# Kernel optimization log

Measured on AMD Instinct MI355X. Metric: run time of the kernel, lower is better.

Reference implementation:

```python
import jax, jax.numpy as jnp
import numpy as np


def setup_inputs() -> dict:
    key = jax.random.key(0)
    kq, kk, kv = jax.random.split(key, 3)
    B, S, D = 8, 2048, 128
    Q = jax.random.normal(kq, (B, S, D), dtype=jnp.float32)
    K = jax.random.normal(kk, (B, S, D), dtype=jnp.float32)
    V = jax.random.normal(kv, (B, S, D), dtype=jnp.float32)
    return {"Q": Q, "K": K, "V": V}


def reference(Q, K, V):
    # scores: [B, S, S]
    d = Q.shape[-1]
    scores = jnp.einsum('bqd,bkd->bqk', Q, K) / jnp.sqrt(jnp.float32(d))
    # causal mask: position i attends to keys <= i (original sets upper triangle to -inf)
    S = scores.shape[-1]
    causal = jnp.tril(jnp.ones((S, S), dtype=bool))  # [S, S]
    scores = jnp.where(causal[None, :, :], scores, -jnp.inf)
    probs = jax.nn.softmax(scores, axis=-1)
    return jnp.einsum('bqk,bkd->bqd', probs, V)
```

## Files before the change

### kernel.cpp

```cpp
#include <hip/hip_runtime.h>

#define BB 8
#define SS 2048
#define DD 128

typedef _Float16 f16;
typedef _Float16 f16x8 __attribute__((ext_vector_type(8)));
typedef float f32x4 __attribute__((ext_vector_type(4)));

#define SWV(d) ((((d) & 7) ^ (((d) >> 3) & 7)) << 3)

static __device__ __forceinline__ unsigned short f2h(float x) {
    f16 h = (f16)x;
    return __builtin_bit_cast(unsigned short, h);
}

static __device__ __forceinline__ float fast_exp2(float x) {
#if __has_builtin(__builtin_amdgcn_exp2f)
    return __builtin_amdgcn_exp2f(x);
#else
    return exp2f(x);
#endif
}

template <int NS>
__global__ __launch_bounds__(256, 2)
void attn_fwd(const float* __restrict__ Qg, const float* __restrict__ Kg,
              const float* __restrict__ Vg, float* __restrict__ Og,
              float* __restrict__ Opart, float2* __restrict__ mlb)
{
    __shared__ __align__(16) f16 Kl[64 * 128];
    __shared__ __align__(16) f16 Vt[128 * 64];
    __shared__ __align__(16) f16 Pl[4][16 * 64];

    const int tid  = threadIdx.x;
    const int lane = tid & 63;
    const int w    = tid >> 6;
    const int c_   = lane & 15;
    const int g    = lane >> 4;

    const int L   = blockIdx.x;
    const int bb  = L & 7;
    const int rem = L >> 3;
    const int qb  = 31 - (rem / NS);
    const int s   = rem % NS;
    const int T   = qb + 1;
    const int t0  = (T * s) / NS;
    const int t1  = (T * (s + 1)) / NS;

    const int qrow0 = qb * 64 + w * 16;

    const float qs = 0.08838834764831845f * 1.4426950408889634f;
    f16x8 qf[4];
    {
        const float* qp = Qg + (size_t)(bb * SS + qrow0 + c_) * DD;
#pragma unroll
        for (int kk = 0; kk < 4; ++kk) {
            const int d0 = kk * 32 + g * 8;
            f32x4 a = *(const f32x4*)(qp + d0);
            f32x4 b = *(const f32x4*)(qp + d0 + 4);
            f16x8 q;
#pragma unroll
            for (int i = 0; i < 4; ++i) {
                q[i]     = (f16)(a[i] * qs);
                q[i + 4] = (f16)(b[i] * qs);
            }
            qf[kk] = q;
        }
    }

    f32x4 Oa[8];
#pragma unroll
    for (int i = 0; i < 8; ++i) Oa[i] = (f32x4){0.f, 0.f, 0.f, 0.f};
    float mrun[4] = {-1e30f, -1e30f, -1e30f, -1e30f};
    float lpart[4] = {0.f, 0.f, 0.f, 0.f};

    f16* Pw = &Pl[w][0];

    const int krow = tid >> 5;
    const int kc4  = tid & 31;
    const int vkg  = tid >> 5;
    const int vq   = tid & 31;

    f32x4 kreg[8], vreg[8];

    if (t0 < t1) {
        {
            const size_t gb = (size_t)(bb * SS + t0 * 64) * DD;
#pragma unroll
            for (int j = 0; j < 8; ++j)
                kreg[j] = *(const f32x4*)(Kg + gb + (krow + 8 * j) * DD + kc4 * 4);
#pragma unroll
            for (int i = 0; i < 8; ++i)
                vreg[i] = *(const f32x4*)(Vg + gb + (vkg * 8 + i) * DD + vq * 4);
        }

        for (int t = t0; t < t1; ++t) {
            __syncthreads();
#pragma unroll
            for (int j = 0; j < 8; ++j) {
                const int row = krow + 8 * j;
                const int el  = row * 128 + ((kc4 * 4) ^ ((row & 7) << 3));
                f32x4 v = kreg[j];
                ushort4 u;
                u.x = f2h(v[0]); u.y = f2h(v[1]); u.z = f2h(v[2]); u.w = f2h(v[3]);
                *(ushort4*)&Kl[el] = u;
            }
#pragma unroll
            for (int dd = 0; dd < 4; ++dd) {
                const int d  = vq * 4 + dd;
                const int sw = SWV(d);
#pragma unroll
                for (int h = 0; h < 2; ++h) {
                    ushort4 u;
                    u.x = f2h(vreg[4 * h + 0][dd]);
                    u.y = f2h(vreg[4 * h + 1][dd]);
                    u.z = f2h(vreg[4 * h + 2][dd]);
                    u.w = f2h(vreg[4 * h + 3][dd]);
                    const int el = d * 64 + ((vkg * 8 + 4 * h) ^ sw);
                    *(ushort4*)&Vt[el] = u;
                }
            }
            __syncthreads();

            if (t + 1 < t1) {
                const size_t gb = (size_t)(bb * SS + (t + 1) * 64) * DD;
#pragma unroll
                for (int j = 0; j < 8; ++j)
                    kreg[j] = *(const f32x4*)(Kg + gb + (krow + 8 * j) * DD + kc4 * 4);
#pragma unroll
                for (int i = 0; i < 8; ++i)
                    vreg[i] = *(const f32x4*)(Vg + gb + (vkg * 8 + i) * DD + vq * 4);
            }

            const int kbase = t * 64;

            f32x4 s4[4];
            __builtin_amdgcn_s_setprio(1);
#pragma unroll
            for (int nb = 0; nb < 4; ++nb) {
                f32x4 acc = (f32x4){0.f, 0.f, 0.f, 0.f};
                const int row = c_ + nb * 16;
                const int sw  = (row & 7) << 3;
#pragma unroll
                for (int kk = 0; kk < 4; ++kk) {
                    f16x8 kb = *(const f16x8*)&Kl[row * 128 + ((kk * 32 + g * 8) ^ sw)];
                    acc = __builtin_amdgcn_mfma_f32_16x16x32_f16(qf[kk], kb, acc, 0, 0, 0);
                }
                s4[nb] = acc;
            }
            __builtin_amdgcn_s_setprio(0);

            if (t == qb) {
#pragma unroll
                for (int nb = 0; nb < 4; ++nb)
#pragma unroll
                    for (int r = 0; r < 4; ++r) {
                        const int kj = kbase + nb * 16 + c_;
                        const int qi = qrow0 + g * 4 + r;
                        if (kj > qi) s4[nb][r] = -1e30f;
                    }
            }

            float pm[4], sc[4];
#pragma unroll
            for (int r = 0; r < 4; ++r) {
                float v = fmaxf(fmaxf(s4[0][r], s4[1][r]), fmaxf(s4[2][r], s4[3][r]));
                v = fmaxf(v, __shfl_xor(v, 1));
                v = fmaxf(v, __shfl_xor(v, 2));
                v = fmaxf(v, __shfl_xor(v, 4));
                v = fmaxf(v, __shfl_xor(v, 8));
                pm[r] = v;
            }
#pragma unroll
            for (int r = 0; r < 4; ++r) {
                const bool keep = (pm[r] - mrun[r] <= 8.0f);
                const float mn  = keep ? mrun[r] : pm[r];
                sc[r]   = keep ? 1.0f : fast_exp2(mrun[r] - pm[r]);
                mrun[r] = mn;
            }
            float rs[4] = {0.f, 0.f, 0.f, 0.f};
            f16 pv16[4][4];
#pragma unroll
            for (int nb = 0; nb < 4; ++nb)
#pragma unroll
                for (int r = 0; r < 4; ++r) {
                    float pv = fast_exp2(s4[nb][r] - mrun[r]);
                    rs[r] += pv;
                    pv16[nb][r] = (f16)pv;
                }
            const float scmin = fminf(fminf(sc[0], sc[1]), fminf(sc[2], sc[3]));
            if (scmin < 1.0f) {
#pragma unroll
                for (int dblk = 0; dblk < 8; ++dblk)
#pragma unroll
                    for (int r = 0; r < 4; ++r) Oa[dblk][r] *= sc[r];
            }
#pragma unroll
            for (int r = 0; r < 4; ++r) lpart[r] = lpart[r] * sc[r] + rs[r];

#pragma unroll
            for (int nb = 0; nb < 4; ++nb)
#pragma unroll
                for (int r = 0; r < 4; ++r) {
                    const int row = g * 4 + r;
                    Pw[row * 64 + ((nb * 16 + c_) ^ ((row & 7) << 3))] = pv16[nb][r];
                }

#pragma unroll
            for (int ks = 0; ks < 2; ++ks) {
                f16x8 pa = *(const f16x8*)&Pw[c_ * 64 + ((ks * 32 + g * 8) ^ ((c_ & 7) << 3))];
                __builtin_amdgcn_s_setprio(1);
#pragma unroll
                for (int dblk = 0; dblk < 8; ++dblk) {
                    const int d  = dblk * 16 + c_;
                    f16x8 vb = *(const f16x8*)&Vt[d * 64 + ((ks * 32 + g * 8) ^ SWV(d))];
                    Oa[dblk] = __builtin_amdgcn_mfma_f32_16x16x32_f16(pa, vb, Oa[dblk], 0, 0, 0);
                }
                __builtin_amdgcn_s_setprio(0);
            }
        }
    }

    float lrun[4];
#pragma unroll
    for (int r = 0; r < 4; ++r) {
        float v = lpart[r];
        v += __shfl_xor(v, 1);
        v += __shfl_xor(v, 2);
        v += __shfl_xor(v, 4);
        v += __shfl_xor(v, 8);
        lrun[r] = v;
    }

    if (NS == 1) {
#pragma unroll
        for (int r = 0; r < 4; ++r) {
            const int qrow = qrow0 + g * 4 + r;
            float* dst = Og + (size_t)(bb * SS + qrow) * DD + c_;
            const float inv = 1.0f / lrun[r];
#pragma unroll
            for (int dblk = 0; dblk < 8; ++dblk) dst[dblk * 16] = Oa[dblk][r] * inv;
        }
    } else {
        float*  od  = (s == 0) ? Og : (Opart + (size_t)(s - 1) * BB * SS * DD);
        float2* mld = mlb + (size_t)s * BB * SS;
#pragma unroll
        for (int r = 0; r < 4; ++r) {
            const int qrow = qrow0 + g * 4 + r;
            float* dst = od + (size_t)(bb * SS + qrow) * DD + c_;
#pragma unroll
            for (int dblk = 0; dblk < 8; ++dblk) dst[dblk * 16] = Oa[dblk][r];
            if (c_ == 0) mld[bb * SS + qrow] = make_float2(mrun[r], lrun[r]);
        }
    }
}

template <int NS>
__global__ __launch_bounds__(256)
void merge_kernel(float* __restrict__ out, const float* __restrict__ Opart,
                  const float2* __restrict__ mlb)
{
    const int idx = blockIdx.x * 256 + threadIdx.x;
    const int row = idx >> 5;
    float2 ml[NS];
#pragma unroll
    for (int i = 0; i < NS; ++i) ml[i] = mlb[(size_t)i * BB * SS + row];
    float mm = ml[0].x;
#pragma unroll
    for (int i = 1; i < NS; ++i) mm = fmaxf(mm, ml[i].x);
    float e[NS], den = 0.f;
#pragma unroll
    for (int i = 0; i < NS; ++i) {
        e[i] = fast_exp2(ml[i].x - mm);
        den += ml[i].y * e[i];
    }
    const float inv = 1.0f / den;
    float4 o = ((const float4*)out)[idx];
    float4 acc;
    acc.x = o.x * e[0]; acc.y = o.y * e[0];
    acc.z = o.z * e[0]; acc.w = o.w * e[0];
#pragma unroll
    for (int i = 1; i < NS; ++i) {
        float4 p = ((const float4*)(Opart + (size_t)(i - 1) * BB * SS * DD))[idx];
        acc.x += p.x * e[i]; acc.y += p.y * e[i];
        acc.z += p.z * e[i]; acc.w += p.w * e[i];
    }
    acc.x *= inv; acc.y *= inv; acc.z *= inv; acc.w *= inv;
    ((float4*)out)[idx] = acc;
}

extern "C" void kernel_launch(void* const* d_in, const int* in_sizes, int n_in,
                              void* d_out, int out_size, void* d_ws, size_t ws_size,
                              hipStream_t stream)
{
    const float* Q = (const float*)d_in[0];
    const float* K = (const float*)d_in[1];
    const float* V = (const float*)d_in[2];
    float* out = (float*)d_out;

    const size_t OB = (size_t)BB * SS * DD * sizeof(float);
    const size_t MB_ = (size_t)BB * SS * sizeof(float2);
    const int mergeGrid = BB * SS * DD / 4 / 256;

    const size_t need4 = 3 * OB + 4 * MB_;
    const size_t need2 = 1 * OB + 2 * MB_;

    if (ws_size >= need4) {
        float*  Op  = (float*)d_ws;
        float2* mlb = (float2*)((char*)d_ws + 3 * OB);
        hipLaunchKernelGGL((attn_fwd<4>), dim3(8 * 32 * 4), dim3(256), 0, stream,
                           Q, K, V, out, Op, mlb);
        hipLaunchKernelGGL((merge_kernel<4>), dim3(mergeGrid), dim3(256), 0, stream,
                           out, Op, mlb);
    } else if (ws_size >= need2) {
        float*  Op  = (float*)d_ws;
        float2* mlb = (float2*)((char*)d_ws + 1 * OB);
        hipLaunchKernelGGL((attn_fwd<2>), dim3(8 * 32 * 2), dim3(256), 0, stream,
                           Q, K, V, out, Op, mlb);
        hipLaunchKernelGGL((merge_kernel<2>), dim3(mergeGrid), dim3(256), 0, stream,
                           out, Op, mlb);
    } else {
        hipLaunchKernelGGL((attn_fwd<1>), dim3(8 * 32), dim3(256), 0, stream,
                           Q, K, V, out, (float*)nullptr, (float2*)nullptr);
    }
}
```

Before: 105.7 us.

## Process two 64-row query tiles per block to reuse staged K/V tiles

Each block now handles 128 query rows: each wave owns two 16-row query tiles that share every K/V tile staged in LDS. This halves how often K/V are loaded and converted per query row, and it halves the grid size. It also swaps scalar f16 conversions for packed cvt_pkrtz and adds a wave-wide fast path that skips rescaling when no row max has grown by more than the threshold. The cost is double the accumulator registers, which may hurt occupancy at launch bounds (256,2), fewer blocks for load balance, and round-toward-zero conversion.

```diff
diff --git a/kernel.cpp b/kernel.cpp
--- a/kernel.cpp
+++ b/kernel.cpp
@@ -5,15 +5,12 @@
 #define DD 128
 
 typedef _Float16 f16;
+typedef _Float16 f16x2 __attribute__((ext_vector_type(2)));
+typedef __fp16 h16x2 __attribute__((ext_vector_type(2)));
 typedef _Float16 f16x8 __attribute__((ext_vector_type(8)));
 typedef float f32x4 __attribute__((ext_vector_type(4)));
 
 #define SWV(d) ((((d) & 7) ^ (((d) >> 3) & 7)) << 3)
-
-static __device__ __forceinline__ unsigned short f2h(float x) {
-    f16 h = (f16)x;
-    return __builtin_bit_cast(unsigned short, h);
-}
 
 static __device__ __forceinline__ float fast_exp2(float x) {
 #if __has_builtin(__builtin_amdgcn_exp2f)
@@ -21,6 +18,20 @@
 #else
     return exp2f(x);
 #endif
+}
+
+static __device__ __forceinline__ f16x2 cvt_pk(float a, float b) {
+    h16x2 r = __builtin_amdgcn_cvt_pkrtz(a, b);
+    return __builtin_bit_cast(f16x2, r);
+}
+
+static __device__ __forceinline__ uint2 pack4(f32x4 v) {
+    f16x2 lo = cvt_pk(v[0], v[1]);
+    f16x2 hi = cvt_pk(v[2], v[3]);
+    uint2 u;
+    u.x = __builtin_bit_cast(unsigned int, lo);
+    u.y = __builtin_bit_cast(unsigned int, hi);
+    return u;
 }
 
 template <int NS>
@@ -31,7 +42,7 @@
 {
     __shared__ __align__(16) f16 Kl[64 * 128];
     __shared__ __align__(16) f16 Vt[128 * 64];
-    __shared__ __align__(16) f16 Pl[4][16 * 64];
+    __shared__ __align__(16) f16 Pl[4][32 * 64];
 
     const int tid  = threadIdx.x;
     const int lane = tid & 63;
@@ -42,18 +53,19 @@
     const int L   = blockIdx.x;
     const int bb  = L & 7;
     const int rem = L >> 3;
-    const int qb  = 31 - (rem / NS);
+    const int qb  = 15 - (rem / NS);
     const int s   = rem % NS;
-    const int T   = qb + 1;
+    const int T   = 2 * qb + 2;
     const int t0  = (T * s) / NS;
     const int t1  = (T * (s + 1)) / NS;
 
-    const int qrow0 = qb * 64 + w * 16;
+    const int qbase = qb * 128 + w * 16;
 
     const float qs = 0.08838834764831845f * 1.4426950408889634f;
-    f16x8 qf[4];
-    {
-        const float* qp = Qg + (size_t)(bb * SS + qrow0 + c_) * DD;
+    f16x8 qf[2][4];
+#pragma unroll
+    for (int rt = 0; rt < 2; ++rt) {
+        const float* qp = Qg + (size_t)(bb * SS + qbase + rt * 64 + c_) * DD;
 #pragma unroll
         for (int kk = 0; kk < 4; ++kk) {
             const int d0 = kk * 32 + g * 8;
@@ -65,15 +77,20 @@
                 q[i]     = (f16)(a[i] * qs);
                 q[i + 4] = (f16)(b[i] * qs);
             }
-            qf[kk] = q;
+            qf[rt][kk] = q;
         }
     }
 
-    f32x4 Oa[8];
-#pragma unroll
-    for (int i = 0; i < 8; ++i) Oa[i] = (f32x4){0.f, 0.f, 0.f, 0.f};
-    float mrun[4] = {-1e30f, -1e30f, -1e30f, -1e30f};
-    float lpart[4] = {0.f, 0.f, 0.f, 0.f};
+    f32x4 Oa[2][8];
+#pragma unroll
+    for (int rt = 0; rt < 2; ++rt)
+#pragma unroll
+        for (int i = 0; i < 8; ++i) Oa[rt][i] = (f32x4){0.f, 0.f, 0.f, 0.f};
+    float mrun[2][4], lpart[2][4];
+#pragma unroll
+    for (int rt = 0; rt < 2; ++rt)
+#pragma unroll
+        for (int r = 0; r < 4; ++r) { mrun[rt][r] = -1e30f; lpart[rt][r] = 0.f; }
 
     f16* Pw = &Pl[w][0];
 
@@ -101,10 +118,7 @@
             for (int j = 0; j < 8; ++j) {
                 const int row = krow + 8 * j;
                 const int el  = row * 128 + ((kc4 * 4) ^ ((row & 7) << 3));
-                f32x4 v = kreg[j];
-                ushort4 u;
-                u.x = f2h(v[0]); u.y = f2h(v[1]); u.z = f2h(v[2]); u.w = f2h(v[3]);
-                *(ushort4*)&Kl[el] = u;
+                *(uint2*)&Kl[el] = pack4(kreg[j]);
             }
 #pragma unroll
             for (int dd = 0; dd < 4; ++dd) {
@@ -112,13 +126,10 @@
                 const int sw = SWV(d);
 #pragma unroll
                 for (int h = 0; h < 2; ++h) {
-                    ushort4 u;
-                    u.x = f2h(vreg[4 * h + 0][dd]);
-                    u.y = f2h(vreg[4 * h + 1][dd]);
-                    u.z = f2h(vreg[4 * h + 2][dd]);
-                    u.w = f2h(vreg[4 * h + 3][dd]);
+                    f32x4 vv = {vreg[4 * h + 0][dd], vreg[4 * h + 1][dd],
+                                vreg[4 * h + 2][dd], vreg[4 * h + 3][dd]};
                     const int el = d * 64 + ((vkg * 8 + 4 * h) ^ sw);
-                    *(ushort4*)&Vt[el] = u;
+                    *(uint2*)&Vt[el] = pack4(vv);
                 }
             }
             __syncthreads();
@@ -133,126 +144,174 @@
                     vreg[i] = *(const f32x4*)(Vg + gb + (vkg * 8 + i) * DD + vq * 4);
             }
 
-            const int kbase = t * 64;
-
-            f32x4 s4[4];
+            f32x4 s4[2][4];
             __builtin_amdgcn_s_setprio(1);
 #pragma unroll
             for (int nb = 0; nb < 4; ++nb) {
-                f32x4 acc = (f32x4){0.f, 0.f, 0.f, 0.f};
                 const int row = c_ + nb * 16;
                 const int sw  = (row & 7) << 3;
-#pragma unroll
-                for (int kk = 0; kk < 4; ++kk) {
-                    f16x8 kb = *(const f16x8*)&Kl[row * 128 + ((kk * 32 + g * 8) ^ sw)];
-                    acc = __builtin_amdgcn_mfma_f32_16x16x32_f16(qf[kk], kb, acc, 0, 0, 0);
-                }
-                s4[nb] = acc;
+                f16x8 kb[4];
+#pragma unroll
+                for (int kk = 0; kk < 4; ++kk)
+                    kb[kk] = *(const f16x8*)&Kl[row * 128 + ((kk * 32 + g * 8) ^ sw)];
+#pragma unroll
+                for (int rt = 0; rt < 2; ++rt) {
+                    f32x4 acc = (f32x4){0.f, 0.f, 0.f, 0.f};
+#pragma unroll
+                    for (int kk = 0; kk < 4; ++kk)
+                        acc = __builtin_amdgcn_mfma_f32_16x16x32_f16(qf[rt][kk], kb[kk], acc, 0, 0, 0);
+                    s4[rt][nb] = acc;
+                }
             }
             __builtin_amdgcn_s_setprio(0);
 
-            if (t == qb) {
-#pragma unroll
-                for (int nb = 0; nb < 4; ++nb)
+            const int kbase = t * 64;
+#pragma unroll
+            for (int rt = 0; rt < 2; ++rt) {
+                if (t >= 2 * qb + rt) {
+#pragma unroll
+                    for (int nb = 0; nb < 4; ++nb)
+#pragma unroll
+                        for (int r = 0; r < 4; ++r) {
+                            const int kj = kbase + nb * 16 + c_;
+                            const int qi = qbase + rt * 64 + g * 4 + r;
+                            if (kj > qi) s4[rt][nb][r] = -1e30f;
+                        }
+                }
+            }
+
+            float wm = -1e30f;
+#pragma unroll
+            for (int rt = 0; rt < 2; ++rt)
+#pragma unroll
+                for (int nb = 0; nb < 4; ++nb) {
+                    f32x4 v = s4[rt][nb];
+                    wm = fmaxf(wm, fmaxf(fmaxf(v[0], v[1]), fmaxf(v[2], v[3])));
+                }
+            wm = fmaxf(wm, __shfl_xor(wm, 1));
+            wm = fmaxf(wm, __shfl_xor(wm, 2));
+            wm = fmaxf(wm, __shfl_xor(wm, 4));
+            wm = fmaxf(wm, __shfl_xor(wm, 8));
+            wm = fmaxf(wm, __shfl_xor(wm, 16));
+            wm = fmaxf(wm, __shfl_xor(wm, 32));
+            float mrmin = 1e30f;
+#pragma unroll
+            for (int rt = 0; rt < 2; ++rt)
+#pragma unroll
+                for (int r = 0; r < 4; ++r) mrmin = fminf(mrmin, mrun[rt][r]);
+
+            if (!__all(wm - mrmin <= 8.0f)) {
+                float sc[2][4];
+                float scmin = 1.0f;
+#pragma unroll
+                for (int rt = 0; rt < 2; ++rt)
 #pragma unroll
                     for (int r = 0; r < 4; ++r) {
-                        const int kj = kbase + nb * 16 + c_;
-                        const int qi = qrow0 + g * 4 + r;
-                        if (kj > qi) s4[nb][r] = -1e30f;
+                        float pm = fmaxf(fmaxf(s4[rt][0][r], s4[rt][1][r]),
+                                         fmaxf(s4[rt][2][r], s4[rt][3][r]));
+                        pm = fmaxf(pm, __shfl_xor(pm, 1));
+                        pm = fmaxf(pm, __shfl_xor(pm, 2));
+                        pm = fmaxf(pm, __shfl_xor(pm, 4));
+                        pm = fmaxf(pm, __shfl_xor(pm, 8));
+                        const bool keep = (pm - mrun[rt][r] <= 8.0f);
+                        sc[rt][r] = keep ? 1.0f : fast_exp2(mrun[rt][r] - pm);
+                        if (!keep) mrun[rt][r] = pm;
+                        scmin = fminf(scmin, sc[rt][r]);
                     }
-            }
-
-            float pm[4], sc[4];
-#pragma unroll
-            for (int r = 0; r < 4; ++r) {
-                float v = fmaxf(fmaxf(s4[0][r], s4[1][r]), fmaxf(s4[2][r], s4[3][r]));
-                v = fmaxf(v, __shfl_xor(v, 1));
-                v = fmaxf(v, __shfl_xor(v, 2));
-                v = fmaxf(v, __shfl_xor(v, 4));
-                v = fmaxf(v, __shfl_xor(v, 8));
-                pm[r] = v;
-            }
-#pragma unroll
-            for (int r = 0; r < 4; ++r) {
-                const bool keep = (pm[r] - mrun[r] <= 8.0f);
-                const float mn  = keep ? mrun[r] : pm[r];
-                sc[r]   = keep ? 1.0f : fast_exp2(mrun[r] - pm[r]);
-                mrun[r] = mn;
-            }
-            float rs[4] = {0.f, 0.f, 0.f, 0.f};
-            f16 pv16[4][4];
-#pragma unroll
-            for (int nb = 0; nb < 4; ++nb)
-#pragma unroll
-                for (int r = 0; r < 4; ++r) {
-                    float pv = fast_exp2(s4[nb][r] - mrun[r]);
-                    rs[r] += pv;
-                    pv16[nb][r] = (f16)pv;
-                }
-            const float scmin = fminf(fminf(sc[0], sc[1]), fminf(sc[2], sc[3]));
-            if (scmin < 1.0f) {
-#pragma unroll
-                for (int dblk = 0; dblk < 8; ++dblk)
-#pragma unroll
-                    for (int r = 0; r < 4; ++r) Oa[dblk][r] *= sc[r];
-            }
-#pragma unroll
-            for (int r = 0; r < 4; ++r) lpart[r] = lpart[r] * sc[r] + rs[r];
-
-#pragma unroll
-            for (int nb = 0; nb < 4; ++nb)
-#pragma unroll
-                for (int r = 0; r < 4; ++r) {
-                    const int row = g * 4 + r;
-                    Pw[row * 64 + ((nb * 16 + c_) ^ ((row & 7) << 3))] = pv16[nb][r];
+                if (scmin < 1.0f) {
+#pragma unroll
+                    for (int rt = 0; rt < 2; ++rt)
+#pragma unroll
+                        for (int r = 0; r < 4; ++r) {
+                            lpart[rt][r] *= sc[rt][r];
+#pragma unroll
+                            for (int dblk = 0; dblk < 8; ++dblk)
+                                Oa[rt][dblk][r] *= sc[rt][r];
+                        }
+                }
+            }
+
+#pragma unroll
+            for (int rt = 0; rt < 2; ++rt)
+#pragma unroll
+                for (int nb = 0; nb < 4; ++nb) {
+                    float pv[4];
+#pragma unroll
+                    for (int r = 0; r < 4; ++r) {
+                        pv[r] = fast_exp2(s4[rt][nb][r] - mrun[rt][r]);
+                        lpart[rt][r] += pv[r];
+                    }
+                    f16x2 p01 = cvt_pk(pv[0], pv[1]);
+                    f16x2 p23 = cvt_pk(pv[2], pv[3]);
+#pragma unroll
+                    for (int r = 0; r < 4; ++r) {
+                        const int row = rt * 16 + g * 4 + r;
+                        const f16 hv = (r < 2) ? p01[r & 1] : p23[r & 1];
+                        Pw[row * 64 + ((nb * 16 + c_) ^ ((row & 7) << 3))] = hv;
+                    }
                 }
 
 #pragma unroll
             for (int ks = 0; ks < 2; ++ks) {
-                f16x8 pa = *(const f16x8*)&Pw[c_ * 64 + ((ks * 32 + g * 8) ^ ((c_ & 7) << 3))];
+                f16x8 pa[2];
+#pragma unroll
+                for (int rt = 0; rt < 2; ++rt) {
+                    const int rr = rt * 16 + c_;
+                    pa[rt] = *(const f16x8*)&Pw[rr * 64 + ((ks * 32 + g * 8) ^ ((c_ & 7) << 3))];
+                }
                 __builtin_amdgcn_s_setprio(1);
 #pragma unroll
                 for (int dblk = 0; dblk < 8; ++dblk) {
                     const int d  = dblk * 16 + c_;
                     f16x8 vb = *(const f16x8*)&Vt[d * 64 + ((ks * 32 + g * 8) ^ SWV(d))];
-                    Oa[dblk] = __builtin_amdgcn_mfma_f32_16x16x32_f16(pa, vb, Oa[dblk], 0, 0, 0);
+#pragma unroll
+                    for (int rt = 0; rt < 2; ++rt)
+                        Oa[rt][dblk] = __builtin_amdgcn_mfma_f32_16x16x32_f16(pa[rt], vb, Oa[rt][dblk], 0, 0, 0);
                 }
                 __builtin_amdgcn_s_setprio(0);
             }
         }
     }
 
-    float lrun[4];
-#pragma unroll
-    for (int r = 0; r < 4; ++r) {
-        float v = lpart[r];
-        v += __shfl_xor(v, 1);
-        v += __shfl_xor(v, 2);
-        v += __shfl_xor(v, 4);
-        v += __shfl_xor(v, 8);
-        lrun[r] = v;
-    }
+    float lrun[2][4];
+#pragma unroll
+    for (int rt = 0; rt < 2; ++rt)
+#pragma unroll
+        for (int r = 0; r < 4; ++r) {
+            float v = lpart[rt][r];
+            v += __shfl_xor(v, 1);
+            v += __shfl_xor(v, 2);
+            v += __shfl_xor(v, 4);
+            v += __shfl_xor(v, 8);
+            lrun[rt][r] = v;
+        }
 
     if (NS == 1) {
 #pragma unroll
-        for (int r = 0; r < 4; ++r) {
-            const int qrow = qrow0 + g * 4 + r;
-            float* dst = Og + (size_t)(bb * SS + qrow) * DD + c_;
-            const float inv = 1.0f / lrun[r];
-#pragma unroll
-            for (int dblk = 0; dblk < 8; ++dblk) dst[dblk * 16] = Oa[dblk][r] * inv;
-        }
+        for (int rt = 0; rt < 2; ++rt)
+#pragma unroll
+            for (int r = 0; r < 4; ++r) {
+                const int qrow = qbase + rt * 64 + g * 4 + r;
+                float* dst = Og + (size_t)(bb * SS + qrow) * DD + c_;
+                const float inv = 1.0f / lrun[rt][r];
+#pragma unroll
+                for (int dblk = 0; dblk < 8; ++dblk)
+                    dst[dblk * 16] = Oa[rt][dblk][r] * inv;
+            }
     } else {
         float*  od  = (s == 0) ? Og : (Opart + (size_t)(s - 1) * BB * SS * DD);
         float2* mld = mlb + (size_t)s * BB * SS;
 #pragma unroll
-        for (int r = 0; r < 4; ++r) {
-            const int qrow = qrow0 + g * 4 + r;
-            float* dst = od + (size_t)(bb * SS + qrow) * DD + c_;
-#pragma unroll
-            for (int dblk = 0; dblk < 8; ++dblk) dst[dblk * 16] = Oa[dblk][r];
-            if (c_ == 0) mld[bb * SS + qrow] = make_float2(mrun[r], lrun[r]);
-        }
+        for (int rt = 0; rt < 2; ++rt)
+#pragma unroll
+            for (int r = 0; r < 4; ++r) {
+                const int qrow = qbase + rt * 64 + g * 4 + r;
+                float* dst = od + (size_t)(bb * SS + qrow) * DD + c_;
+#pragma unroll
+                for (int dblk = 0; dblk < 8; ++dblk)
+                    dst[dblk * 16] = Oa[rt][dblk][r];
+                if (c_ == 0) mld[bb * SS + qrow] = make_float2(mrun[rt][r], lrun[rt][r]);
+            }
     }
 }
 
@@ -299,7 +358,7 @@
     const float* V = (const float*)d_in[2];
     float* out = (float*)d_out;
 
-    const size_t OB = (size_t)BB * SS * DD * sizeof(float);
+    const size_t OB  = (size_t)BB * SS * DD * sizeof(float);
     const size_t MB_ = (size_t)BB * SS * sizeof(float2);
     const int mergeGrid = BB * SS * DD / 4 / 256;
 
@@ -309,19 +368,19 @@
     if (ws_size >= need4) {
         float*  Op  = (float*)d_ws;
         float2* mlb = (float2*)((char*)d_ws + 3 * OB);
-        hipLaunchKernelGGL((attn_fwd<4>), dim3(8 * 32 * 4), dim3(256), 0, stream,
+        hipLaunchKernelGGL((attn_fwd<4>), dim3(8 * 16 * 4), dim3(256), 0, stream,
                            Q, K, V, out, Op, mlb);
         hipLaunchKernelGGL((merge_kernel<4>), dim3(mergeGrid), dim3(256), 0, stream,
                            out, Op, mlb);
     } else if (ws_size >= need2) {
         float*  Op  = (float*)d_ws;
         float2* mlb = (float2*)((char*)d_ws + 1 * OB);
-        hipLaunchKernelGGL((attn_fwd<2>), dim3(8 * 32 * 2), dim3(256), 0, stream,
+        hipLaunchKernelGGL((attn_fwd<2>), dim3(8 * 16 * 2), dim3(256), 0, stream,
                            Q, K, V, out, Op, mlb);
         hipLaunchKernelGGL((merge_kernel<2>), dim3(mergeGrid), dim3(256), 0, stream,
                            out, Op, mlb);
     } else {
-        hipLaunchKernelGGL((attn_fwd<1>), dim3(8 * 32), dim3(256), 0, stream,
+        hipLaunchKernelGGL((attn_fwd<1>), dim3(8 * 16), dim3(256), 0, stream,
                            Q, K, V, out, (float*)nullptr, (float2*)nullptr);
     }
 }
```

New measurement: 157.9 us. 49.3% more time.
